# Kernel tuning notes

Hardware: AMD Instinct MI355X
Metric: run time of the kernel (lower is better)

## Reference

```python
import jax, jax.numpy as jnp
import numpy as np

K = 16            # fixed number of clusters (labels in [0, K))
ALPHA = 1.0
BETA = 1.0
GAMMA = 0.001
VAR_THETA = 0.5
DIST_THETA = 1.5


def setup_inputs() -> dict:
    key = jax.random.key(0)
    k1, k2 = jax.random.split(key)
    B, D, H, W = 8, 32, 512, 512
    embeddings = jax.random.normal(k1, (B, D, H, W), dtype=jnp.float32)
    g_truths = jax.random.randint(k2, (B, H, W), 0, K, dtype=jnp.int32)
    return {"embeddings": embeddings, "g_truths": g_truths}


def _per_image_loss(emb, gt):
    # emb: [D, H, W], gt: [H, W] int32
    D = emb.shape[0]
    x = emb.reshape(D, -1).T              # [N, D] pixels
    lbl = gt.reshape(-1)                  # [N]

    counts = jax.ops.segment_sum(jnp.ones_like(lbl, dtype=x.dtype), lbl, num_segments=K)  # [K]
    counts = jnp.maximum(counts, 1.0)
    sums = jax.ops.segment_sum(x, lbl, num_segments=K)                                    # [K, D]
    means = sums / counts[:, None]                                                        # [K, D]

    # variance (pull) loss: per-cluster mean of hinge^2 on distance to cluster mean
    d2 = jnp.sum((x - means[lbl]) ** 2, axis=-1)         # [N]
    hinge = jnp.maximum(jnp.sqrt(d2) - VAR_THETA, 0.0) ** 2
    per_cluster = jax.ops.segment_sum(hinge, lbl, num_segments=K) / counts
    variance_loss = jnp.mean(per_cluster)

    # distance (push) loss over unordered pairs i<j, normalized by K*(K-1)
    diffs = means[:, None, :] - means[None, :, :]        # [K, K, D]
    sq = jnp.sum(diffs ** 2, axis=-1) + jnp.eye(K, dtype=x.dtype)  # eye guards sqrt(0) on diag
    pd = jnp.sqrt(sq)
    hinge_pd = jnp.maximum(2.0 * DIST_THETA - pd, 0.0) ** 2
    upper = jnp.triu(jnp.ones((K, K), dtype=x.dtype), k=1)
    distance_loss = jnp.sum(hinge_pd * upper) / (K * (K - 1))

    # regularization: mean L2 norm of cluster means
    reg_loss = jnp.mean(jnp.linalg.norm(means, axis=1))

    return ALPHA * variance_loss + BETA * distance_loss + GAMMA * reg_loss


def reference(embeddings, g_truths):
    losses = jax.vmap(_per_image_loss)(embeddings, g_truths)  # [B]
    return jnp.mean(losses)
```

## Files before the change

### kernel.cpp

```cpp
#include <hip/hip_runtime.h>

#define B_IMG 8
#define D_DIM 32
#define NPIX 262144
#define K_CL 16
#define CHUNK 2048
#define CHUNKS (NPIX / CHUNK)
#define PPT 8
#define ACC_STRIDE 272

__device__ __forceinline__ float wave_sum(float v) {
#pragma unroll
  for (int off = 32; off > 0; off >>= 1) v += __shfl_xor(v, off, 64);
  return v;
}

__device__ __forceinline__ void flush_acc(float (*acc)[ACC_STRIDE], int tid,
                                          float* target, int stride) {
  const int w = tid >> 6, lane = tid & 63;
#pragma unroll
  for (int rr = 0; rr < 4; rr++) {
    const int r = (w << 2) | rr;
    float4 v = *(float4*)(&acc[r][lane << 2]);
    *(float4*)(&acc[r][lane << 2]) = make_float4(0.f, 0.f, 0.f, 0.f);
    float tot = wave_sum(v.x + v.y + v.z + v.w);
    if (lane == 0) unsafeAtomicAdd(&target[r * stride], tot);
  }
}

__global__ __launch_bounds__(256) void k_sums(const float* __restrict__ emb,
                                              const int* __restrict__ gt,
                                              float* __restrict__ sums,
                                              float* __restrict__ counts) {
  __shared__ alignas(16) float acc[K_CL][ACC_STRIDE];
  const int tid = threadIdx.x;
  const int b = blockIdx.x >> 7;
  const int chunk = blockIdx.x & (CHUNKS - 1);
  const int base = chunk * CHUNK;

  int lb[PPT];
  {
    const int4* lp = (const int4*)(gt + (size_t)b * NPIX + base);
    int4 a0 = lp[tid];
    int4 a1 = lp[256 + tid];
    lb[0] = a0.x; lb[1] = a0.y; lb[2] = a0.z; lb[3] = a0.w;
    lb[4] = a1.x; lb[5] = a1.y; lb[6] = a1.z; lb[7] = a1.w;
  }
#pragma unroll
  for (int k = 0; k < K_CL; k++) acc[k][tid] = 0.f;
  __syncthreads();

#pragma unroll
  for (int j = 0; j < PPT; j++) acc[lb[j]][tid] += 1.0f;
  __syncthreads();
  flush_acc(acc, tid, counts + b * K_CL, 1);
  __syncthreads();

  for (int d = 0; d < D_DIM; d++) {
    const float4* pp = (const float4*)(emb + ((size_t)b * D_DIM + d) * NPIX + base);
    alignas(16) float v[PPT];
    *(float4*)&v[0] = pp[tid];
    *(float4*)&v[4] = pp[256 + tid];
#pragma unroll
    for (int j = 0; j < PPT; j++) acc[lb[j]][tid] += v[j];
    __syncthreads();
    flush_acc(acc, tid, sums + (size_t)b * K_CL * D_DIM + d, D_DIM);
    __syncthreads();
  }
}

__global__ __launch_bounds__(256) void k_var(const float* __restrict__ emb,
                                             const int* __restrict__ gt,
                                             const float* __restrict__ sums,
                                             const float* __restrict__ counts,
                                             float* __restrict__ var_sums,
                                             float* __restrict__ dist_reg) {
  __shared__ alignas(16) float acc[K_CL][ACC_STRIDE];
  __shared__ float m_lds[D_DIM * K_CL];
  __shared__ float msq[K_CL];
  __shared__ float red4[4];
  const int tid = threadIdx.x;
  const int b = blockIdx.x >> 7;
  const int chunk = blockIdx.x & (CHUNKS - 1);
  const int base = chunk * CHUNK;

  for (int e = tid; e < K_CL * D_DIM; e += 256) {
    const int k = e >> 5, d = e & 31;
    const float c = fmaxf(counts[b * K_CL + k], 1.0f);
    m_lds[d * K_CL + k] = sums[((size_t)b * K_CL + k) * D_DIM + d] / c;
  }
#pragma unroll
  for (int k = 0; k < K_CL; k++) acc[k][tid] = 0.f;
  __syncthreads();
  if (tid < K_CL) {
    float s = 0.f;
#pragma unroll
    for (int d = 0; d < D_DIM; d++) { float m = m_lds[d * K_CL + tid]; s = fmaf(m, m, s); }
    msq[tid] = s;
  }
  __syncthreads();

  if (chunk == 0) {
    const int i = tid >> 4, j = tid & 15;
    float sq = 0.f;
#pragma unroll
    for (int d = 0; d < D_DIM; d++) {
      const float df = m_lds[d * K_CL + i] - m_lds[d * K_CL + j];
      sq = fmaf(df, df, sq);
    }
    float contrib = 0.f;
    if (i < j) {
      const float h = fmaxf(3.0f - sqrtf(sq), 0.0f);
      contrib = h * h;
    }
    const float tot = wave_sum(contrib);
    if ((tid & 63) == 0) red4[tid >> 6] = tot;
    __syncthreads();
    if (tid == 0) {
      const float dist = (red4[0] + red4[1] + red4[2] + red4[3]) * (1.0f / 240.0f);
      float reg = 0.f;
#pragma unroll
      for (int k = 0; k < K_CL; k++) reg += sqrtf(msq[k]);
      dist_reg[b] = dist + 0.001f * (reg * (1.0f / 16.0f));
    }
  }

  int lb[PPT];
  {
    const int4* lp = (const int4*)(gt + (size_t)b * NPIX + base);
    int4 a0 = lp[tid];
    int4 a1 = lp[256 + tid];
    lb[0] = a0.x; lb[1] = a0.y; lb[2] = a0.z; lb[3] = a0.w;
    lb[4] = a1.x; lb[5] = a1.y; lb[6] = a1.z; lb[7] = a1.w;
  }
  float a[PPT];
#pragma unroll
  for (int j = 0; j < PPT; j++) a[j] = 0.f;

  for (int d = 0; d < D_DIM; d++) {
    const float4* pp = (const float4*)(emb + ((size_t)b * D_DIM + d) * NPIX + base);
    alignas(16) float v[PPT];
    *(float4*)&v[0] = pp[tid];
    *(float4*)&v[4] = pp[256 + tid];
    const float* md = &m_lds[d * K_CL];
#pragma unroll
    for (int j = 0; j < PPT; j++) a[j] = fmaf(v[j], v[j] - 2.0f * md[lb[j]], a[j]);
  }
#pragma unroll
  for (int j = 0; j < PPT; j++) {
    const float d2 = a[j] + msq[lb[j]];
    const float dd = sqrtf(fmaxf(d2, 0.f));
    const float h = fmaxf(dd - 0.5f, 0.f);
    acc[lb[j]][tid] += h * h;
  }
  __syncthreads();
  flush_acc(acc, tid, var_sums + b * K_CL, 1);
}

__global__ __launch_bounds__(128) void k_final(const float* __restrict__ counts,
                                               const float* __restrict__ var_sums,
                                               const float* __restrict__ dist_reg,
                                               float* __restrict__ out) {
  const int t = threadIdx.x;
  float pc = 0.f;
  if (t < B_IMG * K_CL) pc = var_sums[t] / fmaxf(counts[t], 1.0f);
#pragma unroll
  for (int off = 8; off > 0; off >>= 1) pc += __shfl_xor(pc, off, 64);
  __shared__ float lb[B_IMG];
  if (t < B_IMG * K_CL && (t & 15) == 0) {
    const int b = t >> 4;
    lb[b] = pc * (1.0f / 16.0f) + dist_reg[b];
  }
  __syncthreads();
  if (t == 0) {
    float s = 0.f;
#pragma unroll
    for (int b = 0; b < B_IMG; b++) s += lb[b];
    out[0] = s * (1.0f / B_IMG);
  }
}

extern "C" void kernel_launch(void* const* d_in, const int* in_sizes, int n_in,
                              void* d_out, int out_size, void* d_ws, size_t ws_size,
                              hipStream_t stream) {
  const float* emb = (const float*)d_in[0];
  const int* gt = (const int*)d_in[1];
  float* out = (float*)d_out;

  float* sums = (float*)d_ws;
  float* counts = sums + B_IMG * K_CL * D_DIM;
  float* var_sums = counts + B_IMG * K_CL;
  float* dist_reg = var_sums + B_IMG * K_CL;

  const size_t ws_floats = B_IMG * K_CL * D_DIM + 2 * B_IMG * K_CL + B_IMG;
  hipMemsetAsync(d_ws, 0, ws_floats * sizeof(float), stream);

  k_sums<<<dim3(B_IMG * CHUNKS), dim3(256), 0, stream>>>(emb, gt, sums, counts);
  k_var<<<dim3(B_IMG * CHUNKS), dim3(256), 0, stream>>>(emb, gt, sums, counts,
                                                        var_sums, dist_reg);
  k_final<<<dim3(1), dim3(128), 0, stream>>>(counts, var_sums, dist_reg, out);
}
```

Measured before the change: 526.6 us.

## Batch four channels per LDS scatter in sums kernel, rebalance chunk sizes

The sums kernel now handles 4096-pixel chunks and accumulates four channels at once into float4 LDS bins. That cuts the number of sync-and-flush rounds from 32 to 8 per block and vectorises both the atomics and the shuffles. The variance kernel switches to 1024-pixel chunks with more blocks and loads cluster means as float4 per cluster, giving one LDS read per four channels. The catch is that the sums kernel now uses about 66KB of LDS, which limits occupancy, and it launches only half as many blocks.

```diff
diff --git a/kernel.cpp b/kernel.cpp
--- a/kernel.cpp
+++ b/kernel.cpp
@@ -4,10 +4,14 @@
 #define D_DIM 32
 #define NPIX 262144
 #define K_CL 16
-#define CHUNK 2048
-#define CHUNKS (NPIX / CHUNK)
-#define PPT 8
-#define ACC_STRIDE 272
+
+#define CHUNK_S 4096
+#define CHUNKS_S (NPIX / CHUNK_S)
+#define AST 257
+
+#define CHUNK_V 1024
+#define CHUNKS_V (NPIX / CHUNK_V)
+#define VST 264
 
 __device__ __forceinline__ float wave_sum(float v) {
 #pragma unroll
@@ -15,16 +19,43 @@
   return v;
 }
 
-__device__ __forceinline__ void flush_acc(float (*acc)[ACC_STRIDE], int tid,
-                                          float* target, int stride) {
+template <int NC>
+__device__ __forceinline__ float4 wave_sum4(float4 v) {
+#pragma unroll
+  for (int off = 32; off > 0; off >>= 1) {
+    v.x += __shfl_xor(v.x, off, 64);
+    if (NC == 4) {
+      v.y += __shfl_xor(v.y, off, 64);
+      v.z += __shfl_xor(v.z, off, 64);
+      v.w += __shfl_xor(v.w, off, 64);
+    }
+  }
+  return v;
+}
+
+template <int NC>
+__device__ __forceinline__ void flush4(float4 (*acc)[AST], int tid,
+                                       float* base, int rstride) {
   const int w = tid >> 6, lane = tid & 63;
 #pragma unroll
   for (int rr = 0; rr < 4; rr++) {
     const int r = (w << 2) | rr;
-    float4 v = *(float4*)(&acc[r][lane << 2]);
-    *(float4*)(&acc[r][lane << 2]) = make_float4(0.f, 0.f, 0.f, 0.f);
-    float tot = wave_sum(v.x + v.y + v.z + v.w);
-    if (lane == 0) unsafeAtomicAdd(&target[r * stride], tot);
+    float4 s = make_float4(0.f, 0.f, 0.f, 0.f);
+#pragma unroll
+    for (int q = 0; q < 4; q++) {
+      float4 v = acc[r][(q << 6) | lane];
+      acc[r][(q << 6) | lane] = make_float4(0.f, 0.f, 0.f, 0.f);
+      s.x += v.x; s.y += v.y; s.z += v.z; s.w += v.w;
+    }
+    s = wave_sum4<NC>(s);
+    if (lane == 0) {
+      unsafeAtomicAdd(base + r * rstride + 0, s.x);
+      if (NC == 4) {
+        unsafeAtomicAdd(base + r * rstride + 1, s.y);
+        unsafeAtomicAdd(base + r * rstride + 2, s.z);
+        unsafeAtomicAdd(base + r * rstride + 3, s.w);
+      }
+    }
   }
 }
 
@@ -32,39 +63,55 @@
                                               const int* __restrict__ gt,
                                               float* __restrict__ sums,
                                               float* __restrict__ counts) {
-  __shared__ alignas(16) float acc[K_CL][ACC_STRIDE];
+  __shared__ float4 acc4[K_CL][AST];
   const int tid = threadIdx.x;
-  const int b = blockIdx.x >> 7;
-  const int chunk = blockIdx.x & (CHUNKS - 1);
-  const int base = chunk * CHUNK;
-
-  int lb[PPT];
+  const int b = blockIdx.x >> 6;
+  const int chunk = blockIdx.x & (CHUNKS_S - 1);
+  const int base = chunk * CHUNK_S;
+
+  int lb[16];
   {
     const int4* lp = (const int4*)(gt + (size_t)b * NPIX + base);
-    int4 a0 = lp[tid];
-    int4 a1 = lp[256 + tid];
-    lb[0] = a0.x; lb[1] = a0.y; lb[2] = a0.z; lb[3] = a0.w;
-    lb[4] = a1.x; lb[5] = a1.y; lb[6] = a1.z; lb[7] = a1.w;
-  }
-#pragma unroll
-  for (int k = 0; k < K_CL; k++) acc[k][tid] = 0.f;
-  __syncthreads();
-
-#pragma unroll
-  for (int j = 0; j < PPT; j++) acc[lb[j]][tid] += 1.0f;
-  __syncthreads();
-  flush_acc(acc, tid, counts + b * K_CL, 1);
-  __syncthreads();
-
-  for (int d = 0; d < D_DIM; d++) {
-    const float4* pp = (const float4*)(emb + ((size_t)b * D_DIM + d) * NPIX + base);
-    alignas(16) float v[PPT];
-    *(float4*)&v[0] = pp[tid];
-    *(float4*)&v[4] = pp[256 + tid];
-#pragma unroll
-    for (int j = 0; j < PPT; j++) acc[lb[j]][tid] += v[j];
+#pragma unroll
+    for (int h = 0; h < 4; h++) {
+      int4 a = lp[tid + (h << 8)];
+      lb[h * 4 + 0] = a.x; lb[h * 4 + 1] = a.y;
+      lb[h * 4 + 2] = a.z; lb[h * 4 + 3] = a.w;
+    }
+  }
+#pragma unroll
+  for (int k = 0; k < K_CL; k++) acc4[k][tid] = make_float4(0.f, 0.f, 0.f, 0.f);
+  __syncthreads();
+
+#pragma unroll
+  for (int j = 0; j < 16; j++) acc4[lb[j]][tid].x += 1.0f;
+  __syncthreads();
+  flush4<1>(acc4, tid, counts + b * K_CL, 1);
+  __syncthreads();
+
+  for (int g = 0; g < 8; g++) {
+    const float* eb = emb + ((size_t)b * D_DIM + g * 4) * NPIX + base;
+#pragma unroll
+    for (int h = 0; h < 4; h++) {
+      float4 v[4];
+#pragma unroll
+      for (int d = 0; d < 4; d++)
+        v[d] = ((const float4*)(eb + (size_t)d * NPIX))[tid + (h << 8)];
+#pragma unroll
+      for (int c = 0; c < 4; c++) {
+        const int l = lb[h * 4 + c];
+        float4 t;
+        t.x = ((const float*)&v[0])[c];
+        t.y = ((const float*)&v[1])[c];
+        t.z = ((const float*)&v[2])[c];
+        t.w = ((const float*)&v[3])[c];
+        float4 old = acc4[l][tid];
+        old.x += t.x; old.y += t.y; old.z += t.z; old.w += t.w;
+        acc4[l][tid] = old;
+      }
+    }
     __syncthreads();
-    flush_acc(acc, tid, sums + (size_t)b * K_CL * D_DIM + d, D_DIM);
+    flush4<4>(acc4, tid, sums + (size_t)b * K_CL * D_DIM + g * 4, D_DIM);
     __syncthreads();
   }
 }
@@ -75,19 +122,22 @@
                                              const float* __restrict__ counts,
                                              float* __restrict__ var_sums,
                                              float* __restrict__ dist_reg) {
-  __shared__ alignas(16) float acc[K_CL][ACC_STRIDE];
-  __shared__ float m_lds[D_DIM * K_CL];
+  __shared__ float acc[K_CL][VST];
+  __shared__ float4 mk4[K_CL][9];
   __shared__ float msq[K_CL];
   __shared__ float red4[4];
   const int tid = threadIdx.x;
-  const int b = blockIdx.x >> 7;
-  const int chunk = blockIdx.x & (CHUNKS - 1);
-  const int base = chunk * CHUNK;
-
-  for (int e = tid; e < K_CL * D_DIM; e += 256) {
+  const int b = blockIdx.x >> 8;
+  const int chunk = blockIdx.x & (CHUNKS_V - 1);
+  const int base = chunk * CHUNK_V;
+
+  float* mkf = (float*)mk4;
+#pragma unroll
+  for (int e0 = 0; e0 < 2; e0++) {
+    const int e = tid + (e0 << 8);
     const int k = e >> 5, d = e & 31;
     const float c = fmaxf(counts[b * K_CL + k], 1.0f);
-    m_lds[d * K_CL + k] = sums[((size_t)b * K_CL + k) * D_DIM + d] / c;
+    mkf[k * 36 + d] = sums[(size_t)b * K_CL * D_DIM + e] / c;
   }
 #pragma unroll
   for (int k = 0; k < K_CL; k++) acc[k][tid] = 0.f;
@@ -95,7 +145,11 @@
   if (tid < K_CL) {
     float s = 0.f;
 #pragma unroll
-    for (int d = 0; d < D_DIM; d++) { float m = m_lds[d * K_CL + tid]; s = fmaf(m, m, s); }
+    for (int g = 0; g < 8; g++) {
+      float4 m = mk4[tid][g];
+      s = fmaf(m.x, m.x, s); s = fmaf(m.y, m.y, s);
+      s = fmaf(m.z, m.z, s); s = fmaf(m.w, m.w, s);
+    }
     msq[tid] = s;
   }
   __syncthreads();
@@ -104,9 +158,11 @@
     const int i = tid >> 4, j = tid & 15;
     float sq = 0.f;
 #pragma unroll
-    for (int d = 0; d < D_DIM; d++) {
-      const float df = m_lds[d * K_CL + i] - m_lds[d * K_CL + j];
-      sq = fmaf(df, df, sq);
+    for (int g = 0; g < 8; g++) {
+      float4 mi = mk4[i][g], mj = mk4[j][g];
+      float dx = mi.x - mj.x, dy = mi.y - mj.y, dz = mi.z - mj.z, dw = mi.w - mj.w;
+      sq = fmaf(dx, dx, sq); sq = fmaf(dy, dy, sq);
+      sq = fmaf(dz, dz, sq); sq = fmaf(dw, dw, sq);
     }
     float contrib = 0.f;
     if (i < j) {
@@ -125,36 +181,49 @@
     }
   }
 
-  int lb[PPT];
+  int lb[4];
   {
     const int4* lp = (const int4*)(gt + (size_t)b * NPIX + base);
-    int4 a0 = lp[tid];
-    int4 a1 = lp[256 + tid];
-    lb[0] = a0.x; lb[1] = a0.y; lb[2] = a0.z; lb[3] = a0.w;
-    lb[4] = a1.x; lb[5] = a1.y; lb[6] = a1.z; lb[7] = a1.w;
-  }
-  float a[PPT];
-#pragma unroll
-  for (int j = 0; j < PPT; j++) a[j] = 0.f;
-
-  for (int d = 0; d < D_DIM; d++) {
-    const float4* pp = (const float4*)(emb + ((size_t)b * D_DIM + d) * NPIX + base);
-    alignas(16) float v[PPT];
-    *(float4*)&v[0] = pp[tid];
-    *(float4*)&v[4] = pp[256 + tid];
-    const float* md = &m_lds[d * K_CL];
-#pragma unroll
-    for (int j = 0; j < PPT; j++) a[j] = fmaf(v[j], v[j] - 2.0f * md[lb[j]], a[j]);
-  }
-#pragma unroll
-  for (int j = 0; j < PPT; j++) {
+    int4 a = lp[tid];
+    lb[0] = a.x; lb[1] = a.y; lb[2] = a.z; lb[3] = a.w;
+  }
+  float a[4] = {0.f, 0.f, 0.f, 0.f};
+
+#pragma unroll 2
+  for (int g = 0; g < 8; g++) {
+    const float* eb = emb + ((size_t)b * D_DIM + g * 4) * NPIX + base;
+    float4 v[4];
+#pragma unroll
+    for (int d = 0; d < 4; d++)
+      v[d] = ((const float4*)(eb + (size_t)d * NPIX))[tid];
+#pragma unroll
+    for (int j = 0; j < 4; j++) {
+      const float4 m4 = mk4[lb[j]][g];
+#pragma unroll
+      for (int d = 0; d < 4; d++) {
+        const float x = ((const float*)&v[d])[j];
+        const float mm = ((const float*)&m4)[d];
+        a[j] = fmaf(x, x - 2.0f * mm, a[j]);
+      }
+    }
+  }
+#pragma unroll
+  for (int j = 0; j < 4; j++) {
     const float d2 = a[j] + msq[lb[j]];
     const float dd = sqrtf(fmaxf(d2, 0.f));
     const float h = fmaxf(dd - 0.5f, 0.f);
     acc[lb[j]][tid] += h * h;
   }
   __syncthreads();
-  flush_acc(acc, tid, var_sums + b * K_CL, 1);
+
+  const int w = tid >> 6, lane = tid & 63;
+#pragma unroll
+  for (int rr = 0; rr < 4; rr++) {
+    const int r = (w << 2) | rr;
+    float4 vv = *(float4*)(&acc[r][lane << 2]);
+    float tot = wave_sum(vv.x + vv.y + vv.z + vv.w);
+    if (lane == 0) unsafeAtomicAdd(&var_sums[b * K_CL + r], tot);
+  }
 }
 
 __global__ __launch_bounds__(128) void k_final(const float* __restrict__ counts,
@@ -166,16 +235,16 @@
   if (t < B_IMG * K_CL) pc = var_sums[t] / fmaxf(counts[t], 1.0f);
 #pragma unroll
   for (int off = 8; off > 0; off >>= 1) pc += __shfl_xor(pc, off, 64);
-  __shared__ float lb[B_IMG];
+  __shared__ float lbl[B_IMG];
   if (t < B_IMG * K_CL && (t & 15) == 0) {
     const int b = t >> 4;
-    lb[b] = pc * (1.0f / 16.0f) + dist_reg[b];
+    lbl[b] = pc * (1.0f / 16.0f) + dist_reg[b];
   }
   __syncthreads();
   if (t == 0) {
     float s = 0.f;
 #pragma unroll
-    for (int b = 0; b < B_IMG; b++) s += lb[b];
+    for (int b = 0; b < B_IMG; b++) s += lbl[b];
     out[0] = s * (1.0f / B_IMG);
   }
 }
@@ -195,8 +264,8 @@
   const size_t ws_floats = B_IMG * K_CL * D_DIM + 2 * B_IMG * K_CL + B_IMG;
   hipMemsetAsync(d_ws, 0, ws_floats * sizeof(float), stream);
 
-  k_sums<<<dim3(B_IMG * CHUNKS), dim3(256), 0, stream>>>(emb, gt, sums, counts);
-  k_var<<<dim3(B_IMG * CHUNKS), dim3(256), 0, stream>>>(emb, gt, sums, counts,
-                                                        var_sums, dist_reg);
+  k_sums<<<dim3(B_IMG * CHUNKS_S), dim3(256), 0, stream>>>(emb, gt, sums, counts);
+  k_var<<<dim3(B_IMG * CHUNKS_V), dim3(256), 0, stream>>>(emb, gt, sums, counts,
+                                                          var_sums, dist_reg);
   k_final<<<dim3(1), dim3(128), 0, stream>>>(counts, var_sums, dist_reg, out);
 }
```

After: 573.6 us. 1.09x slower.

## Replace per-dimension block reductions with LDS atomic binning and a means kernel

Applied to the files above, without the earlier changes.

k_sums no longer runs a barrier, wave reduction and global atomic flush for each of the 32 dimensions. Each thread now does LDS atomic adds into 16-way replicated bins per cluster and dimension, followed by a single final reduction. Mean computation and the distance/reg terms move into a small k_means kernel, so k_var only loads precomputed means. k_var also software-pipelines its embedding loads with nontemporal hints. The trade-off is heavier LDS atomic traffic and one extra kernel launch.

```diff
diff --git a/kernel.cpp b/kernel.cpp
--- a/kernel.cpp
+++ b/kernel.cpp
@@ -6,39 +6,36 @@
 #define K_CL 16
 #define CHUNK 2048
 #define CHUNKS (NPIX / CHUNK)
-#define PPT 8
-#define ACC_STRIDE 272
+#define F4_D (NPIX / 4)
+
+typedef float f4 __attribute__((ext_vector_type(4)));
 
 __device__ __forceinline__ float wave_sum(float v) {
 #pragma unroll
   for (int off = 32; off > 0; off >>= 1) v += __shfl_xor(v, off, 64);
   return v;
-}
-
-__device__ __forceinline__ void flush_acc(float (*acc)[ACC_STRIDE], int tid,
-                                          float* target, int stride) {
-  const int w = tid >> 6, lane = tid & 63;
-#pragma unroll
-  for (int rr = 0; rr < 4; rr++) {
-    const int r = (w << 2) | rr;
-    float4 v = *(float4*)(&acc[r][lane << 2]);
-    *(float4*)(&acc[r][lane << 2]) = make_float4(0.f, 0.f, 0.f, 0.f);
-    float tot = wave_sum(v.x + v.y + v.z + v.w);
-    if (lane == 0) unsafeAtomicAdd(&target[r * stride], tot);
-  }
 }
 
 __global__ __launch_bounds__(256) void k_sums(const float* __restrict__ emb,
                                               const int* __restrict__ gt,
                                               float* __restrict__ sums,
                                               float* __restrict__ counts) {
-  __shared__ alignas(16) float acc[K_CL][ACC_STRIDE];
+  __shared__ float bins[K_CL][D_DIM][16];
+  __shared__ float cnt[K_CL][16];
   const int tid = threadIdx.x;
   const int b = blockIdx.x >> 7;
   const int chunk = blockIdx.x & (CHUNKS - 1);
   const int base = chunk * CHUNK;
-
-  int lb[PPT];
+  const int col = tid & 15;
+
+  {
+    f4* bz = (f4*)bins;
+#pragma unroll
+    for (int i = 0; i < 8; i++) bz[tid + (i << 8)] = (f4)0.f;
+    if (tid < 64) ((f4*)cnt)[tid] = (f4)0.f;
+  }
+
+  int lb[8];
   {
     const int4* lp = (const int4*)(gt + (size_t)b * NPIX + base);
     int4 a0 = lp[tid];
@@ -46,86 +43,126 @@
     lb[0] = a0.x; lb[1] = a0.y; lb[2] = a0.z; lb[3] = a0.w;
     lb[4] = a1.x; lb[5] = a1.y; lb[6] = a1.z; lb[7] = a1.w;
   }
-#pragma unroll
-  for (int k = 0; k < K_CL; k++) acc[k][tid] = 0.f;
-  __syncthreads();
-
-#pragma unroll
-  for (int j = 0; j < PPT; j++) acc[lb[j]][tid] += 1.0f;
-  __syncthreads();
-  flush_acc(acc, tid, counts + b * K_CL, 1);
-  __syncthreads();
-
+  __syncthreads();
+
+#pragma unroll
+  for (int j = 0; j < 8; j++) atomicAdd(&cnt[lb[j]][col], 1.0f);
+
+  for (int g = 0; g < 8; g++) {
+    const f4* eb = (const f4*)(emb + ((size_t)b * D_DIM + g * 4) * NPIX + base);
+#pragma unroll
+    for (int h = 0; h < 2; h++) {
+      f4 v0 = __builtin_nontemporal_load(&eb[(size_t)0 * F4_D + tid + (h << 8)]);
+      f4 v1 = __builtin_nontemporal_load(&eb[(size_t)1 * F4_D + tid + (h << 8)]);
+      f4 v2 = __builtin_nontemporal_load(&eb[(size_t)2 * F4_D + tid + (h << 8)]);
+      f4 v3 = __builtin_nontemporal_load(&eb[(size_t)3 * F4_D + tid + (h << 8)]);
+#pragma unroll
+      for (int c = 0; c < 4; c++) {
+        const int l = lb[(h << 2) | c];
+        atomicAdd(&bins[l][g * 4 + 0][col], v0[c]);
+        atomicAdd(&bins[l][g * 4 + 1][col], v1[c]);
+        atomicAdd(&bins[l][g * 4 + 2][col], v2[c]);
+        atomicAdd(&bins[l][g * 4 + 3][col], v3[c]);
+      }
+    }
+  }
+  __syncthreads();
+
+#pragma unroll
+  for (int p0 = 0; p0 < 2; p0++) {
+    const int p = tid + (p0 << 8);
+    const f4* r = (const f4*)bins[p >> 5][p & 31];
+    f4 s0 = r[0], s1 = r[1], s2 = r[2], s3 = r[3];
+    const float tot = (s0[0] + s0[1] + s0[2] + s0[3]) + (s1[0] + s1[1] + s1[2] + s1[3]) +
+                      (s2[0] + s2[1] + s2[2] + s2[3]) + (s3[0] + s3[1] + s3[2] + s3[3]);
+    unsafeAtomicAdd(&sums[(size_t)b * K_CL * D_DIM + p], tot);
+  }
+  if (tid < K_CL) {
+    const f4* r = (const f4*)cnt[tid];
+    f4 s0 = r[0], s1 = r[1], s2 = r[2], s3 = r[3];
+    const float tot = (s0[0] + s0[1] + s0[2] + s0[3]) + (s1[0] + s1[1] + s1[2] + s1[3]) +
+                      (s2[0] + s2[1] + s2[2] + s2[3]) + (s3[0] + s3[1] + s3[2] + s3[3]);
+    unsafeAtomicAdd(&counts[b * K_CL + tid], tot);
+  }
+}
+
+__global__ __launch_bounds__(256) void k_means(const float* __restrict__ sums,
+                                               const float* __restrict__ counts,
+                                               float* __restrict__ mt,
+                                               float* __restrict__ msq_g,
+                                               float* __restrict__ dist_reg) {
+  __shared__ float mm[K_CL][33];
+  __shared__ float msq_s[K_CL];
+  __shared__ float red4[4];
+  const int b = blockIdx.x;
+  const int t = threadIdx.x;
+
+#pragma unroll
+  for (int e0 = 0; e0 < 2; e0++) {
+    const int e = t + (e0 << 8);
+    const int k = e >> 5, d = e & 31;
+    const float c = fmaxf(counts[b * K_CL + k], 1.0f);
+    const float m = sums[(size_t)b * K_CL * D_DIM + e] / c;
+    mm[k][d] = m;
+    mt[(size_t)b * D_DIM * K_CL + d * K_CL + k] = m;
+  }
+  __syncthreads();
+  if (t < K_CL) {
+    float s = 0.f;
+#pragma unroll
+    for (int d = 0; d < D_DIM; d++) { const float m = mm[t][d]; s = fmaf(m, m, s); }
+    msq_s[t] = s;
+    msq_g[b * K_CL + t] = s;
+  }
+  __syncthreads();
+
+  const int i = t >> 4, j = t & 15;
+  float sq = 0.f;
+#pragma unroll
   for (int d = 0; d < D_DIM; d++) {
-    const float4* pp = (const float4*)(emb + ((size_t)b * D_DIM + d) * NPIX + base);
-    alignas(16) float v[PPT];
-    *(float4*)&v[0] = pp[tid];
-    *(float4*)&v[4] = pp[256 + tid];
-#pragma unroll
-    for (int j = 0; j < PPT; j++) acc[lb[j]][tid] += v[j];
-    __syncthreads();
-    flush_acc(acc, tid, sums + (size_t)b * K_CL * D_DIM + d, D_DIM);
-    __syncthreads();
+    const float df = mm[i][d] - mm[j][d];
+    sq = fmaf(df, df, sq);
+  }
+  float contrib = 0.f;
+  if (i < j) {
+    const float h = fmaxf(3.0f - sqrtf(sq), 0.0f);
+    contrib = h * h;
+  }
+  const float tot = wave_sum(contrib);
+  if ((t & 63) == 0) red4[t >> 6] = tot;
+  __syncthreads();
+  if (t == 0) {
+    const float dist = (red4[0] + red4[1] + red4[2] + red4[3]) * (1.0f / 240.0f);
+    float reg = 0.f;
+#pragma unroll
+    for (int k = 0; k < K_CL; k++) reg += sqrtf(msq_s[k]);
+    dist_reg[b] = dist + 0.001f * (reg * (1.0f / 16.0f));
   }
 }
 
 __global__ __launch_bounds__(256) void k_var(const float* __restrict__ emb,
                                              const int* __restrict__ gt,
-                                             const float* __restrict__ sums,
-                                             const float* __restrict__ counts,
-                                             float* __restrict__ var_sums,
-                                             float* __restrict__ dist_reg) {
-  __shared__ alignas(16) float acc[K_CL][ACC_STRIDE];
-  __shared__ float m_lds[D_DIM * K_CL];
+                                             const float* __restrict__ mt,
+                                             const float* __restrict__ msq_g,
+                                             float* __restrict__ var_sums) {
+  __shared__ float tm[D_DIM][K_CL];
   __shared__ float msq[K_CL];
-  __shared__ float red4[4];
+  __shared__ float vacc[K_CL][16];
   const int tid = threadIdx.x;
   const int b = blockIdx.x >> 7;
   const int chunk = blockIdx.x & (CHUNKS - 1);
   const int base = chunk * CHUNK;
-
-  for (int e = tid; e < K_CL * D_DIM; e += 256) {
-    const int k = e >> 5, d = e & 31;
-    const float c = fmaxf(counts[b * K_CL + k], 1.0f);
-    m_lds[d * K_CL + k] = sums[((size_t)b * K_CL + k) * D_DIM + d] / c;
-  }
-#pragma unroll
-  for (int k = 0; k < K_CL; k++) acc[k][tid] = 0.f;
-  __syncthreads();
-  if (tid < K_CL) {
-    float s = 0.f;
-#pragma unroll
-    for (int d = 0; d < D_DIM; d++) { float m = m_lds[d * K_CL + tid]; s = fmaf(m, m, s); }
-    msq[tid] = s;
-  }
-  __syncthreads();
-
-  if (chunk == 0) {
-    const int i = tid >> 4, j = tid & 15;
-    float sq = 0.f;
-#pragma unroll
-    for (int d = 0; d < D_DIM; d++) {
-      const float df = m_lds[d * K_CL + i] - m_lds[d * K_CL + j];
-      sq = fmaf(df, df, sq);
-    }
-    float contrib = 0.f;
-    if (i < j) {
-      const float h = fmaxf(3.0f - sqrtf(sq), 0.0f);
-      contrib = h * h;
-    }
-    const float tot = wave_sum(contrib);
-    if ((tid & 63) == 0) red4[tid >> 6] = tot;
-    __syncthreads();
-    if (tid == 0) {
-      const float dist = (red4[0] + red4[1] + red4[2] + red4[3]) * (1.0f / 240.0f);
-      float reg = 0.f;
-#pragma unroll
-      for (int k = 0; k < K_CL; k++) reg += sqrtf(msq[k]);
-      dist_reg[b] = dist + 0.001f * (reg * (1.0f / 16.0f));
-    }
-  }
-
-  int lb[PPT];
+  const int col = tid & 15;
+
+#pragma unroll
+  for (int e0 = 0; e0 < 2; e0++) {
+    const int e = tid + (e0 << 8);
+    ((float*)tm)[e] = 2.0f * mt[(size_t)b * D_DIM * K_CL + e];
+  }
+  if (tid < K_CL) msq[tid] = msq_g[b * K_CL + tid];
+  ((float*)vacc)[tid] = 0.f;
+
+  int lb[8];
   {
     const int4* lp = (const int4*)(gt + (size_t)b * NPIX + base);
     int4 a0 = lp[tid];
@@ -133,28 +170,66 @@
     lb[0] = a0.x; lb[1] = a0.y; lb[2] = a0.z; lb[3] = a0.w;
     lb[4] = a1.x; lb[5] = a1.y; lb[6] = a1.z; lb[7] = a1.w;
   }
-  float a[PPT];
-#pragma unroll
-  for (int j = 0; j < PPT; j++) a[j] = 0.f;
-
-  for (int d = 0; d < D_DIM; d++) {
-    const float4* pp = (const float4*)(emb + ((size_t)b * D_DIM + d) * NPIX + base);
-    alignas(16) float v[PPT];
-    *(float4*)&v[0] = pp[tid];
-    *(float4*)&v[4] = pp[256 + tid];
-    const float* md = &m_lds[d * K_CL];
-#pragma unroll
-    for (int j = 0; j < PPT; j++) a[j] = fmaf(v[j], v[j] - 2.0f * md[lb[j]], a[j]);
-  }
-#pragma unroll
-  for (int j = 0; j < PPT; j++) {
+  __syncthreads();
+
+  float a[8] = {0.f, 0.f, 0.f, 0.f, 0.f, 0.f, 0.f, 0.f};
+  const f4* P = (const f4*)(emb + (size_t)b * D_DIM * NPIX + base);
+
+  f4 A0 = __builtin_nontemporal_load(&P[tid]);
+  f4 B0 = __builtin_nontemporal_load(&P[256 + tid]);
+  f4 A1 = __builtin_nontemporal_load(&P[(size_t)F4_D + tid]);
+  f4 B1 = __builtin_nontemporal_load(&P[(size_t)F4_D + 256 + tid]);
+
+  for (int d = 0; d < D_DIM; d += 2) {
+    {
+      const float* td = tm[d];
+#pragma unroll
+      for (int j = 0; j < 4; j++) {
+        const float x = A0[j];
+        a[j] = fmaf(x, x - td[lb[j]], a[j]);
+      }
+#pragma unroll
+      for (int j = 0; j < 4; j++) {
+        const float x = B0[j];
+        a[4 + j] = fmaf(x, x - td[lb[4 + j]], a[4 + j]);
+      }
+      const int dn = (d + 2) & 31;
+      A0 = __builtin_nontemporal_load(&P[(size_t)dn * F4_D + tid]);
+      B0 = __builtin_nontemporal_load(&P[(size_t)dn * F4_D + 256 + tid]);
+    }
+    {
+      const float* te = tm[d + 1];
+#pragma unroll
+      for (int j = 0; j < 4; j++) {
+        const float x = A1[j];
+        a[j] = fmaf(x, x - te[lb[j]], a[j]);
+      }
+#pragma unroll
+      for (int j = 0; j < 4; j++) {
+        const float x = B1[j];
+        a[4 + j] = fmaf(x, x - te[lb[4 + j]], a[4 + j]);
+      }
+      const int dm = (d + 3) & 31;
+      A1 = __builtin_nontemporal_load(&P[(size_t)dm * F4_D + tid]);
+      B1 = __builtin_nontemporal_load(&P[(size_t)dm * F4_D + 256 + tid]);
+    }
+  }
+
+#pragma unroll
+  for (int j = 0; j < 8; j++) {
     const float d2 = a[j] + msq[lb[j]];
     const float dd = sqrtf(fmaxf(d2, 0.f));
     const float h = fmaxf(dd - 0.5f, 0.f);
-    acc[lb[j]][tid] += h * h;
-  }
-  __syncthreads();
-  flush_acc(acc, tid, var_sums + b * K_CL, 1);
+    atomicAdd(&vacc[lb[j]][col], h * h);
+  }
+  __syncthreads();
+  if (tid < K_CL) {
+    const f4* r = (const f4*)vacc[tid];
+    f4 s0 = r[0], s1 = r[1], s2 = r[2], s3 = r[3];
+    const float tot = (s0[0] + s0[1] + s0[2] + s0[3]) + (s1[0] + s1[1] + s1[2] + s1[3]) +
+                      (s2[0] + s2[1] + s2[2] + s2[3]) + (s3[0] + s3[1] + s3[2] + s3[3]);
+    unsafeAtomicAdd(&var_sums[b * K_CL + tid], tot);
+  }
 }
 
 __global__ __launch_bounds__(128) void k_final(const float* __restrict__ counts,
@@ -166,16 +241,16 @@
   if (t < B_IMG * K_CL) pc = var_sums[t] / fmaxf(counts[t], 1.0f);
 #pragma unroll
   for (int off = 8; off > 0; off >>= 1) pc += __shfl_xor(pc, off, 64);
-  __shared__ float lb[B_IMG];
+  __shared__ float lbl[B_IMG];
   if (t < B_IMG * K_CL && (t & 15) == 0) {
     const int b = t >> 4;
-    lb[b] = pc * (1.0f / 16.0f) + dist_reg[b];
+    lbl[b] = pc * (1.0f / 16.0f) + dist_reg[b];
   }
   __syncthreads();
   if (t == 0) {
     float s = 0.f;
 #pragma unroll
-    for (int b = 0; b < B_IMG; b++) s += lb[b];
+    for (int b = 0; b < B_IMG; b++) s += lbl[b];
     out[0] = s * (1.0f / B_IMG);
   }
 }
@@ -191,12 +266,14 @@
   float* counts = sums + B_IMG * K_CL * D_DIM;
   float* var_sums = counts + B_IMG * K_CL;
   float* dist_reg = var_sums + B_IMG * K_CL;
-
-  const size_t ws_floats = B_IMG * K_CL * D_DIM + 2 * B_IMG * K_CL + B_IMG;
-  hipMemsetAsync(d_ws, 0, ws_floats * sizeof(float), stream);
+  float* mt = dist_reg + B_IMG;
+  float* msq_g = mt + B_IMG * D_DIM * K_CL;
+
+  const size_t zero_floats = B_IMG * K_CL * D_DIM + 2 * B_IMG * K_CL + B_IMG;
+  (void)hipMemsetAsync(d_ws, 0, zero_floats * sizeof(float), stream);
 
   k_sums<<<dim3(B_IMG * CHUNKS), dim3(256), 0, stream>>>(emb, gt, sums, counts);
-  k_var<<<dim3(B_IMG * CHUNKS), dim3(256), 0, stream>>>(emb, gt, sums, counts,
-                                                        var_sums, dist_reg);
+  k_means<<<dim3(B_IMG), dim3(256), 0, stream>>>(sums, counts, mt, msq_g, dist_reg);
+  k_var<<<dim3(B_IMG * CHUNKS), dim3(256), 0, stream>>>(emb, gt, mt, msq_g, var_sums);
   k_final<<<dim3(1), dim3(128), 0, stream>>>(counts, var_sums, dist_reg, out);
 }
```

Result: slower. 690.7 us (+31.1%).
